# Kernel tuning notes

Hardware: AMD Instinct MI355X
Metric: run time of the kernel (lower is better)

Reference implementation:

```python
import jax, jax.numpy as jnp
import numpy as np

BLOCK_LEN = 64


def segsum(x):
    """x: (..., T) -> (..., T, T) with segsum[i,j] = sum_{k=j+1..i} x[k] (lower-tri incl diag), -inf above."""
    T = x.shape[-1]
    xc = jnp.cumsum(x, axis=-1)
    seg = xc[..., :, None] - xc[..., None, :]
    mask = jnp.tril(jnp.ones((T, T), dtype=bool))
    return jnp.where(mask, seg, -jnp.inf)


def setup_inputs() -> dict:
    key = jax.random.key(0)
    kx, ka, kb, kc = jax.random.split(key, 4)
    b, s, h, p, n = 4, 4096, 32, 64, 64
    X = jax.random.normal(kx, (b, s, h), dtype=jnp.float32)  # placeholder to keep split order stable
    X = jax.random.normal(kx, (b, s, h, p), dtype=jnp.float32)
    # A must be negative for a stable SSM decay (exp of cumulative sums stays bounded)
    A = -jax.random.uniform(ka, (b, s, h), dtype=jnp.float32, minval=0.0, maxval=1.0)
    B = jax.random.normal(kb, (b, s, h, n), dtype=jnp.float32)
    C = jax.random.normal(kc, (b, s, h, n), dtype=jnp.float32)
    return {"X": X, "A": A, "B": B, "C": C}


def reference(X, A, B, C):
    blk = BLOCK_LEN
    b, s, h, p = X.shape
    n = B.shape[-1]
    c = s // blk
    # chunk: b (c l) ... -> b c l ...
    Xc = X.reshape(b, c, blk, h, p)
    Bc = B.reshape(b, c, blk, h, n)
    Cc = C.reshape(b, c, blk, h, n)
    Ac = A.reshape(b, c, blk, h).transpose(0, 3, 1, 2)  # b h c l
    A_cumsum = jnp.cumsum(Ac, axis=-1)                  # b h c l

    # 1. intra-chunk (diagonal block) output
    L = jnp.exp(segsum(Ac))                             # b h c l s
    Y_diag = jnp.einsum("bclhn,bcshn,bhcls,bcshp->bclhp", Cc, Bc, L, Xc)

    # 2. intra-chunk states (chunk-final state assuming zero initial state)
    decay_states = jnp.exp(A_cumsum[..., -1:] - A_cumsum)
    states = jnp.einsum("bclhn,bhcl,bclhp->bchpn", Bc, decay_states, Xc)

    # 3. inter-chunk recurrence over chunk boundaries
    init = jnp.zeros_like(states[:, :1])
    states = jnp.concatenate([init, states], axis=1)    # b (c+1) h p n
    A_last = jnp.pad(A_cumsum[..., -1], ((0, 0), (0, 0), (1, 0)))  # b h (c+1)
    decay_chunk = jnp.exp(segsum(A_last))               # b h (c+1) (c+1)
    new_states = jnp.einsum("bhzc,bchpn->bzhpn", decay_chunk, states)
    states_in = new_states[:, :-1]                      # state entering each chunk

    # 4. state -> output
    state_decay_out = jnp.exp(A_cumsum)
    Y_off = jnp.einsum("bclhn,bchpn,bhcl->bclhp", Cc, states_in, state_decay_out)

    Y = (Y_diag + Y_off).reshape(b, s, h, p)
    return Y
```

## Files before the change

### kernel.cpp

```cpp
#include <hip/hip_runtime.h>

namespace {

typedef __attribute__((ext_vector_type(8))) short short8;
typedef __attribute__((ext_vector_type(4))) float f32x4;

constexpr int Hh = 32;
constexpr int Ss = 4096;
constexpr int HP = 64;
constexpr int HN = 64;
constexpr int NCH = 64;
constexpr int SB = 72;
constexpr int SS = 68;

__device__ inline unsigned short f2bf(float f) {
  unsigned u = __float_as_uint(f);
  u += 0x7FFFu + ((u >> 16) & 1u);
  return (unsigned short)(u >> 16);
}
__device__ inline float bf2f(unsigned short s) {
  return __uint_as_float(((unsigned)s) << 16);
}

__global__ __launch_bounds__(512, 1)
void ssd_mfma(const float* __restrict__ Xg0, const float* __restrict__ Ag0,
              const float* __restrict__ Bg0, const float* __restrict__ Cg0,
              float* __restrict__ Yg0) {
  __shared__ unsigned short Cs[2][64 * SB];
  __shared__ unsigned short Bs[2][64 * SB];
  __shared__ unsigned short BT[2][64 * SB];
  __shared__ unsigned short XT[2][32 * SB];
  __shared__ unsigned short Gs[64 * SB];
  __shared__ float STs[32 * SS];
  __shared__ float ac[2][64];

  const int tid = threadIdx.x;
  const int blk = blockIdx.x;
  const int ph = blk & 1;
  const int hi = (blk >> 1) & 31;
  const int bi = blk >> 6;

  const float* Xg = Xg0 + ((size_t)bi * Ss * Hh + hi) * HP + ph * 32;
  const float* Bg = Bg0 + ((size_t)bi * Ss * Hh + hi) * HN;
  const float* Cg = Cg0 + ((size_t)bi * Ss * Hh + hi) * HN;
  const float* Ag = Ag0 + (size_t)bi * Ss * Hh + hi;
  float*       Yg = Yg0 + ((size_t)bi * Ss * Hh + hi) * HP + ph * 32;

  const int w = tid >> 6, lane = tid & 63;
  const int lr = lane & 15, lk = lane >> 4;

  for (int i = tid; i < 32 * SS; i += 512) STs[i] = 0.f;

  float4 rb0, rb1, rc0, rc1, rx0;

  auto stage_load = [&](int ci) {
    const size_t rB = (size_t)ci * 64;
    const int r = tid >> 4, c = (tid & 15) * 4;
    rb0 = *(const float4*)(Bg + (rB + r) * (Hh * HN) + c);
    rc0 = *(const float4*)(Cg + (rB + r) * (Hh * HN) + c);
    rb1 = *(const float4*)(Bg + (rB + r + 32) * (Hh * HN) + c);
    rc1 = *(const float4*)(Cg + (rB + r + 32) * (Hh * HN) + c);
    const int rx = tid >> 3, cx = (tid & 7) * 4;
    rx0 = *(const float4*)(Xg + (rB + rx) * (Hh * HP) + cx);
  };

  auto stage_write = [&](int buf) {
    unsigned short* bs = Bs[buf];
    unsigned short* cs = Cs[buf];
    unsigned short* bt = BT[buf];
    unsigned short* xt = XT[buf];
    const int r = tid >> 4, c = (tid & 15) * 4;
    unsigned short b0[4] = {f2bf(rb0.x), f2bf(rb0.y), f2bf(rb0.z), f2bf(rb0.w)};
    unsigned short b1[4] = {f2bf(rb1.x), f2bf(rb1.y), f2bf(rb1.z), f2bf(rb1.w)};
    unsigned short c0[4] = {f2bf(rc0.x), f2bf(rc0.y), f2bf(rc0.z), f2bf(rc0.w)};
    unsigned short c1[4] = {f2bf(rc1.x), f2bf(rc1.y), f2bf(rc1.z), f2bf(rc1.w)};
    *(uint2*)&bs[r * SB + c]        = *(const uint2*)b0;
    *(uint2*)&bs[(r + 32) * SB + c] = *(const uint2*)b1;
    *(uint2*)&cs[r * SB + c]        = *(const uint2*)c0;
    *(uint2*)&cs[(r + 32) * SB + c] = *(const uint2*)c1;
#pragma unroll
    for (int j = 0; j < 4; ++j) {
      bt[(c + j) * SB + r]      = b0[j];
      bt[(c + j) * SB + r + 32] = b1[j];
    }
    const int rx = tid >> 3, cx = (tid & 7) * 4;
    unsigned short x0[4] = {f2bf(rx0.x), f2bf(rx0.y), f2bf(rx0.z), f2bf(rx0.w)};
#pragma unroll
    for (int j = 0; j < 4; ++j) xt[(cx + j) * SB + rx] = x0[j];
  };

  auto a_scan = [&](int ci) {
    if (tid < 64) {
      float a = Ag[(size_t)(ci * 64 + tid) * Hh];
#pragma unroll
      for (int off = 1; off < 64; off <<= 1) {
        float v = __shfl_up(a, off);
        if (tid >= off) a += v;
      }
      ac[ci & 1][tid] = a;
    }
  };

  stage_load(0);
  stage_write(0);
  a_scan(0);

  for (int ci = 0; ci < NCH; ++ci) {
    const int cur = ci & 1;
    __syncthreads();

    if (ci + 1 < NCH) {
      stage_load(ci + 1);
      a_scan(ci + 1);
    }

    const unsigned short* cs = Cs[cur];
    const unsigned short* bs = Bs[cur];
    const unsigned short* bt = BT[cur];
    const unsigned short* xt = XT[cur];
    const float* acv = ac[cur];
    const size_t rB = (size_t)ci * 64;

    {
      const int tl = w >> 1;
#pragma unroll
      for (int t = 0; t < 2; ++t) {
        const int ts = (w & 1) * 2 + t;
        if (ts > tl) {
#pragma unroll
          for (int i = 0; i < 4; ++i)
            Gs[(tl * 16 + lk * 4 + i) * SB + ts * 16 + lr] = 0;
        } else {
          f32x4 acc = {0.f, 0.f, 0.f, 0.f};
#pragma unroll
          for (int ks = 0; ks < 2; ++ks) {
            short8 a = *(const short8*)&cs[(tl * 16 + lr) * SB + ks * 32 + lk * 8];
            short8 b = *(const short8*)&bs[(ts * 16 + lr) * SB + ks * 32 + lk * 8];
            acc = __builtin_amdgcn_mfma_f32_16x16x32_bf16(a, b, acc, 0, 0, 0);
          }
          const int gcol = ts * 16 + lr;
          const float acol = acv[gcol];
#pragma unroll
          for (int i = 0; i < 4; ++i) {
            const int grow = tl * 16 + lk * 4 + i;
            float g = (gcol <= grow) ? acc[i] * __expf(acv[grow] - acol) : 0.f;
            Gs[grow * SB + gcol] = f2bf(g);
          }
        }
      }
    }
    __syncthreads();

    {
      const int tl = w >> 1, tp = w & 1;
      f32x4 aD = {0.f, 0.f, 0.f, 0.f};
      f32x4 aO = {0.f, 0.f, 0.f, 0.f};
#pragma unroll
      for (int ks = 0; ks < 2; ++ks) {
        const int ko = ks * 32 + lk * 8;
        short8 g = *(const short8*)&Gs[(tl * 16 + lr) * SB + ko];
        short8 x = *(const short8*)&xt[(tp * 16 + lr) * SB + ko];
        aD = __builtin_amdgcn_mfma_f32_16x16x32_bf16(g, x, aD, 0, 0, 0);
        short8 c8 = *(const short8*)&cs[(tl * 16 + lr) * SB + ko];
        const float* srow = &STs[(tp * 16 + lr) * SS + ko];
        float4 s0 = *(const float4*)srow;
        float4 s1 = *(const float4*)(srow + 4);
        short8 sb;
        sb[0] = (short)f2bf(s0.x); sb[1] = (short)f2bf(s0.y);
        sb[2] = (short)f2bf(s0.z); sb[3] = (short)f2bf(s0.w);
        sb[4] = (short)f2bf(s1.x); sb[5] = (short)f2bf(s1.y);
        sb[6] = (short)f2bf(s1.z); sb[7] = (short)f2bf(s1.w);
        aO = __builtin_amdgcn_mfma_f32_16x16x32_bf16(c8, sb, aO, 0, 0, 0);
      }
#pragma unroll
      for (int i = 0; i < 4; ++i) {
        const int grow = tl * 16 + lk * 4 + i;
        const float el = __expf(acv[grow]);
        Yg[(rB + grow) * (Hh * HP) + tp * 16 + lr] = aD[i] + el * aO[i];
      }
    }
    __syncthreads();

    {
      const int tp = w >> 2, tn = w & 3;
      const float atot = acv[63];
      f32x4 acc = {0.f, 0.f, 0.f, 0.f};
#pragma unroll
      for (int ks = 0; ks < 2; ++ks) {
        const int ko = ks * 32 + lk * 8;
        short8 a = *(const short8*)&xt[(tp * 16 + lr) * SB + ko];
        short8 braw = *(const short8*)&bt[(tn * 16 + lr) * SB + ko];
        short8 bsc;
#pragma unroll
        for (int j = 0; j < 8; ++j) {
          const float dl = __expf(atot - acv[ko + j]);
          bsc[j] = (short)f2bf(bf2f((unsigned short)braw[j]) * dl);
        }
        acc = __builtin_amdgcn_mfma_f32_16x16x32_bf16(a, bsc, acc, 0, 0, 0);
      }
      const float ea = __expf(atot);
#pragma unroll
      for (int i = 0; i < 4; ++i) {
        const int p = tp * 16 + lk * 4 + i, n = tn * 16 + lr;
        STs[p * SS + n] = STs[p * SS + n] * ea + acc[i];
      }
    }

    if (ci + 1 < NCH) stage_write((ci + 1) & 1);
  }
}

}

extern "C" void kernel_launch(void* const* d_in, const int* in_sizes, int n_in,
                              void* d_out, int out_size, void* d_ws, size_t ws_size,
                              hipStream_t stream) {
  const float* X = (const float*)d_in[0];
  const float* A = (const float*)d_in[1];
  const float* B = (const float*)d_in[2];
  const float* C = (const float*)d_in[3];
  float* Y = (float*)d_out;
  (void)d_ws; (void)ws_size; (void)in_sizes; (void)n_in; (void)out_size;
  ssd_mfma<<<dim3(256), dim3(512), 0, stream>>>(X, A, B, C, Y);
}
```

Baseline: 236.7 us.

## Split warps into diag and state-update groups with prescaled B and register state

```diff
diff --git a/kernel.cpp b/kernel.cpp
--- a/kernel.cpp
+++ b/kernel.cpp
@@ -5,40 +5,50 @@
 typedef __attribute__((ext_vector_type(8))) short short8;
 typedef __attribute__((ext_vector_type(4))) float f32x4;
 
-constexpr int Hh = 32;
-constexpr int Ss = 4096;
-constexpr int HP = 64;
-constexpr int HN = 64;
-constexpr int NCH = 64;
-constexpr int SB = 72;
-constexpr int SS = 68;
+constexpr int Hh = 32, Ss = 4096, HP = 64, HN = 64, NCH = 64;
+constexpr int ST = 68;
 
 __device__ inline unsigned short f2bf(float f) {
   unsigned u = __float_as_uint(f);
   u += 0x7FFFu + ((u >> 16) & 1u);
   return (unsigned short)(u >> 16);
 }
-__device__ inline float bf2f(unsigned short s) {
-  return __uint_as_float(((unsigned)s) << 16);
-}
-
-__global__ __launch_bounds__(512, 1)
-void ssd_mfma(const float* __restrict__ Xg0, const float* __restrict__ Ag0,
-              const float* __restrict__ Bg0, const float* __restrict__ Cg0,
-              float* __restrict__ Yg0) {
-  __shared__ unsigned short Cs[2][64 * SB];
-  __shared__ unsigned short Bs[2][64 * SB];
-  __shared__ unsigned short BT[2][64 * SB];
-  __shared__ unsigned short XT[2][32 * SB];
-  __shared__ unsigned short Gs[64 * SB];
-  __shared__ float STs[32 * SS];
-  __shared__ float ac[2][64];
+
+__device__ inline short8 frag(const unsigned short* p) {
+  union { short8 s; uint2 u[2]; } r;
+  r.u[0] = *(const uint2*)p;
+  r.u[1] = *(const uint2*)(p + 4);
+  return r.s;
+}
+
+__device__ inline uint2 cvt4(float4 v) {
+  uint2 o; unsigned short* s = (unsigned short*)&o;
+  s[0] = f2bf(v.x); s[1] = f2bf(v.y); s[2] = f2bf(v.z); s[3] = f2bf(v.w);
+  return o;
+}
+
+__device__ inline uint2 sxor8(uint2 v) {
+  uint2 o;
+  o.x = (unsigned)__shfl_xor((int)v.x, 8);
+  o.y = (unsigned)__shfl_xor((int)v.y, 8);
+  return o;
+}
+
+__global__ __launch_bounds__(1024, 4)
+void ssd4(const float* __restrict__ Xg0, const float* __restrict__ Ag0,
+          const float* __restrict__ Bg0, const float* __restrict__ Cg0,
+          float* __restrict__ Yg0) {
+  __shared__ unsigned short Bs[2][64 * ST];
+  __shared__ unsigned short Cs[2][64 * ST];
+  __shared__ unsigned short BT[2][64 * ST];
+  __shared__ unsigned short XT[2][32 * ST];
+  __shared__ unsigned short Gs[64 * ST];
+  __shared__ unsigned short Sb[2][32 * ST];
+  __shared__ float elt[4][64], ielt[4][64];
 
   const int tid = threadIdx.x;
-  const int blk = blockIdx.x;
-  const int ph = blk & 1;
-  const int hi = (blk >> 1) & 31;
-  const int bi = blk >> 6;
+  const int blk = ((blockIdx.x & 7) << 5) | (blockIdx.x >> 3);
+  const int ph = blk & 1, hi = (blk >> 1) & 31, bi = blk >> 6;
 
   const float* Xg = Xg0 + ((size_t)bi * Ss * Hh + hi) * HP + ph * 32;
   const float* Bg = Bg0 + ((size_t)bi * Ss * Hh + hi) * HN;
@@ -49,45 +59,14 @@
   const int w = tid >> 6, lane = tid & 63;
   const int lr = lane & 15, lk = lane >> 4;
 
-  for (int i = tid; i < 32 * SS; i += 512) STs[i] = 0.f;
-
-  float4 rb0, rb1, rc0, rc1, rx0;
-
-  auto stage_load = [&](int ci) {
-    const size_t rB = (size_t)ci * 64;
-    const int r = tid >> 4, c = (tid & 15) * 4;
-    rb0 = *(const float4*)(Bg + (rB + r) * (Hh * HN) + c);
-    rc0 = *(const float4*)(Cg + (rB + r) * (Hh * HN) + c);
-    rb1 = *(const float4*)(Bg + (rB + r + 32) * (Hh * HN) + c);
-    rc1 = *(const float4*)(Cg + (rB + r + 32) * (Hh * HN) + c);
-    const int rx = tid >> 3, cx = (tid & 7) * 4;
-    rx0 = *(const float4*)(Xg + (rB + rx) * (Hh * HP) + cx);
-  };
-
-  auto stage_write = [&](int buf) {
-    unsigned short* bs = Bs[buf];
-    unsigned short* cs = Cs[buf];
-    unsigned short* bt = BT[buf];
-    unsigned short* xt = XT[buf];
-    const int r = tid >> 4, c = (tid & 15) * 4;
-    unsigned short b0[4] = {f2bf(rb0.x), f2bf(rb0.y), f2bf(rb0.z), f2bf(rb0.w)};
-    unsigned short b1[4] = {f2bf(rb1.x), f2bf(rb1.y), f2bf(rb1.z), f2bf(rb1.w)};
-    unsigned short c0[4] = {f2bf(rc0.x), f2bf(rc0.y), f2bf(rc0.z), f2bf(rc0.w)};
-    unsigned short c1[4] = {f2bf(rc1.x), f2bf(rc1.y), f2bf(rc1.z), f2bf(rc1.w)};
-    *(uint2*)&bs[r * SB + c]        = *(const uint2*)b0;
-    *(uint2*)&bs[(r + 32) * SB + c] = *(const uint2*)b1;
-    *(uint2*)&cs[r * SB + c]        = *(const uint2*)c0;
-    *(uint2*)&cs[(r + 32) * SB + c] = *(const uint2*)c1;
-#pragma unroll
-    for (int j = 0; j < 4; ++j) {
-      bt[(c + j) * SB + r]      = b0[j];
-      bt[(c + j) * SB + r + 32] = b1[j];
-    }
-    const int rx = tid >> 3, cx = (tid & 7) * 4;
-    unsigned short x0[4] = {f2bf(rx0.x), f2bf(rx0.y), f2bf(rx0.z), f2bf(rx0.w)};
-#pragma unroll
-    for (int j = 0; j < 4; ++j) xt[(cx + j) * SB + rx] = x0[j];
-  };
+  const int tlA[8] = {0, 1, 1, 2, 2, 2, 3, 3};
+  const int tsA[8] = {0, 0, 1, 0, 1, 2, 0, 2};
+  const int ntA[8] = {1, 1, 1, 1, 1, 1, 2, 2};
+
+  for (int i = tid; i < 64 * ST; i += 1024) Gs[i] = 0;
+  for (int i = tid; i < 32 * ST; i += 1024) { Sb[0][i] = 0; Sb[1][i] = 0; }
+
+  float4 rA, rB2, rC1, rC2;
 
   auto a_scan = [&](int ci) {
     if (tid < 64) {
@@ -97,116 +76,149 @@
         float v = __shfl_up(a, off);
         if (tid >= off) a += v;
       }
-      ac[ci & 1][tid] = a;
+      elt[ci & 3][tid] = __expf(a);
+      ielt[ci & 3][tid] = __expf(-a);
     }
   };
 
+  auto stage_load = [&](int ci) {
+    const size_t rowB = (size_t)ci * 64;
+    if (w >= 8) {
+      const int u = tid - 512;
+      const int r = u >> 3, c = (u & 7) * 4;
+      const float* bp = Bg + (rowB + r) * (size_t)(Hh * HN);
+      const float* cp = Cg + (rowB + r) * (size_t)(Hh * HN);
+      rA  = *(const float4*)(bp + c);
+      rB2 = *(const float4*)(bp + c + 32);
+      rC1 = *(const float4*)(cp + c);
+      rC2 = *(const float4*)(cp + c + 32);
+    } else {
+      const int r = tid >> 3, c = (tid & 7) * 4;
+      rA = *(const float4*)(Xg + (rowB + r) * (size_t)(Hh * HP) + c);
+    }
+  };
+
+  auto stage_write = [&](int ci) {
+    const int buf = ci & 1, nb = ci & 3;
+    if (w >= 8) {
+      const int u = tid - 512;
+      const int r = u >> 3, c = (u & 7) * 4;
+      const float sc = ielt[nb][r];
+      float4 s1 = rA;  s1.x *= sc; s1.y *= sc; s1.z *= sc; s1.w *= sc;
+      float4 s2 = rB2; s2.x *= sc; s2.y *= sc; s2.z *= sc; s2.w *= sc;
+      uint2 t1 = cvt4(s1), t2 = cvt4(s2);
+      *(uint2*)&Bs[buf][r * ST + c]      = t1;
+      *(uint2*)&Bs[buf][r * ST + c + 32] = t2;
+      *(uint2*)&Cs[buf][r * ST + c]      = cvt4(rC1);
+      *(uint2*)&Cs[buf][r * ST + c + 32] = cvt4(rC2);
+      uint2 u1 = sxor8(t1), u2 = sxor8(t2);
+      const unsigned short* m1 = (const unsigned short*)&t1;
+      const unsigned short* p1 = (const unsigned short*)&u1;
+      const unsigned short* m2 = (const unsigned short*)&t2;
+      const unsigned short* p2 = (const unsigned short*)&u2;
+      const int g = r & 1, re = r & ~1;
+#pragma unroll
+      for (int jj = 0; jj < 2; ++jj) {
+        const int j = g * 2 + jj;
+        unsigned lo1 = g ? p1[j] : m1[j], hi1 = g ? m1[j] : p1[j];
+        unsigned lo2 = g ? p2[j] : m2[j], hi2 = g ? m2[j] : p2[j];
+        *(unsigned*)&BT[buf][(c + j) * ST + re]      = lo1 | (hi1 << 16);
+        *(unsigned*)&BT[buf][(c + 32 + j) * ST + re] = lo2 | (hi2 << 16);
+      }
+    } else {
+      const int r = tid >> 3, c = (tid & 7) * 4;
+      uint2 t1 = cvt4(rA);
+      uint2 u1 = sxor8(t1);
+      const unsigned short* m1 = (const unsigned short*)&t1;
+      const unsigned short* p1 = (const unsigned short*)&u1;
+      const int g = r & 1, re = r & ~1;
+#pragma unroll
+      for (int jj = 0; jj < 2; ++jj) {
+        const int j = g * 2 + jj;
+        unsigned lo = g ? p1[j] : m1[j], hi = g ? m1[j] : p1[j];
+        *(unsigned*)&XT[buf][(c + j) * ST + re] = lo | (hi << 16);
+      }
+    }
+  };
+
+  a_scan(0);
+  a_scan(1);
+  __syncthreads();
   stage_load(0);
   stage_write(0);
-  a_scan(0);
+  f32x4 Sreg = {0.f, 0.f, 0.f, 0.f};
 
   for (int ci = 0; ci < NCH; ++ci) {
     const int cur = ci & 1;
     __syncthreads();
-
-    if (ci + 1 < NCH) {
-      stage_load(ci + 1);
-      a_scan(ci + 1);
-    }
-
-    const unsigned short* cs = Cs[cur];
-    const unsigned short* bs = Bs[cur];
-    const unsigned short* bt = BT[cur];
-    const unsigned short* xt = XT[cur];
-    const float* acv = ac[cur];
-    const size_t rB = (size_t)ci * 64;
-
-    {
-      const int tl = w >> 1;
+    if (ci + 1 < NCH) stage_load(ci + 1);
+    if (ci + 2 < NCH) a_scan(ci + 2);
+
+    if (w < 8) {
+      const int tl = tlA[w];
+      const float* el = elt[ci & 3];
 #pragma unroll
       for (int t = 0; t < 2; ++t) {
-        const int ts = (w & 1) * 2 + t;
-        if (ts > tl) {
-#pragma unroll
-          for (int i = 0; i < 4; ++i)
-            Gs[(tl * 16 + lk * 4 + i) * SB + ts * 16 + lr] = 0;
-        } else {
-          f32x4 acc = {0.f, 0.f, 0.f, 0.f};
-#pragma unroll
-          for (int ks = 0; ks < 2; ++ks) {
-            short8 a = *(const short8*)&cs[(tl * 16 + lr) * SB + ks * 32 + lk * 8];
-            short8 b = *(const short8*)&bs[(ts * 16 + lr) * SB + ks * 32 + lk * 8];
-            acc = __builtin_amdgcn_mfma_f32_16x16x32_bf16(a, b, acc, 0, 0, 0);
-          }
-          const int gcol = ts * 16 + lr;
-          const float acol = acv[gcol];
-#pragma unroll
-          for (int i = 0; i < 4; ++i) {
-            const int grow = tl * 16 + lk * 4 + i;
-            float g = (gcol <= grow) ? acc[i] * __expf(acv[grow] - acol) : 0.f;
-            Gs[grow * SB + gcol] = f2bf(g);
-          }
+        if (t >= ntA[w]) break;
+        const int ts = tsA[w] + t;
+        f32x4 acc = {0.f, 0.f, 0.f, 0.f};
+#pragma unroll
+        for (int ks = 0; ks < 2; ++ks) {
+          short8 a = frag(&Cs[cur][(tl * 16 + lr) * ST + ks * 32 + lk * 8]);
+          short8 b = frag(&Bs[cur][(ts * 16 + lr) * ST + ks * 32 + lk * 8]);
+          acc = __builtin_amdgcn_mfma_f32_16x16x32_bf16(a, b, acc, 0, 0, 0);
         }
-      }
-    }
+        const int gcol = ts * 16 + lr;
+#pragma unroll
+        for (int i = 0; i < 4; ++i) {
+          const int grow = tl * 16 + lk * 4 + i;
+          float gv = (gcol <= grow) ? acc[i] * el[grow] : 0.f;
+          Gs[grow * ST + gcol] = f2bf(gv);
+        }
+      }
+    } else {
+      const int u = w - 8, tp = u >> 2, tn = u & 3;
+      f32x4 acc = Sreg;
+#pragma unroll
+      for (int ks = 0; ks < 2; ++ks) {
+        short8 a = frag(&XT[cur][(tp * 16 + lr) * ST + ks * 32 + lk * 8]);
+        short8 b = frag(&BT[cur][(tn * 16 + lr) * ST + ks * 32 + lk * 8]);
+        acc = __builtin_amdgcn_mfma_f32_16x16x32_bf16(a, b, acc, 0, 0, 0);
+      }
+      const float ea = elt[ci & 3][63];
+#pragma unroll
+      for (int i = 0; i < 4; ++i) acc[i] *= ea;
+      Sreg = acc;
+#pragma unroll
+      for (int i = 0; i < 4; ++i)
+        Sb[(ci + 1) & 1][(tp * 16 + lk * 4 + i) * ST + tn * 16 + lr] = f2bf(acc[i]);
+    }
+
     __syncthreads();
 
-    {
+    if (w < 8) {
       const int tl = w >> 1, tp = w & 1;
-      f32x4 aD = {0.f, 0.f, 0.f, 0.f};
-      f32x4 aO = {0.f, 0.f, 0.f, 0.f};
+      const size_t rB0 = (size_t)ci * 64;
+      f32x4 aD = {0.f, 0.f, 0.f, 0.f}, aO = {0.f, 0.f, 0.f, 0.f};
 #pragma unroll
       for (int ks = 0; ks < 2; ++ks) {
         const int ko = ks * 32 + lk * 8;
-        short8 g = *(const short8*)&Gs[(tl * 16 + lr) * SB + ko];
-        short8 x = *(const short8*)&xt[(tp * 16 + lr) * SB + ko];
-        aD = __builtin_amdgcn_mfma_f32_16x16x32_bf16(g, x, aD, 0, 0, 0);
-        short8 c8 = *(const short8*)&cs[(tl * 16 + lr) * SB + ko];
-        const float* srow = &STs[(tp * 16 + lr) * SS + ko];
-        float4 s0 = *(const float4*)srow;
-        float4 s1 = *(const float4*)(srow + 4);
-        short8 sb;
-        sb[0] = (short)f2bf(s0.x); sb[1] = (short)f2bf(s0.y);
-        sb[2] = (short)f2bf(s0.z); sb[3] = (short)f2bf(s0.w);
-        sb[4] = (short)f2bf(s1.x); sb[5] = (short)f2bf(s1.y);
-        sb[6] = (short)f2bf(s1.z); sb[7] = (short)f2bf(s1.w);
-        aO = __builtin_amdgcn_mfma_f32_16x16x32_bf16(c8, sb, aO, 0, 0, 0);
-      }
+        short8 gf = frag(&Gs[(tl * 16 + lr) * ST + ko]);
+        short8 xf = frag(&XT[cur][(tp * 16 + lr) * ST + ko]);
+        aD = __builtin_amdgcn_mfma_f32_16x16x32_bf16(gf, xf, aD, 0, 0, 0);
+        short8 cf = frag(&Cs[cur][(tl * 16 + lr) * ST + ko]);
+        short8 sf = frag(&Sb[cur][(tp * 16 + lr) * ST + ko]);
+        aO = __builtin_amdgcn_mfma_f32_16x16x32_bf16(cf, sf, aO, 0, 0, 0);
+      }
+      const float* el = elt[ci & 3];
 #pragma unroll
       for (int i = 0; i < 4; ++i) {
-        const int grow = tl * 16 + lk * 4 + i;
-        const float el = __expf(acv[grow]);
-        Yg[(rB + grow) * (Hh * HP) + tp * 16 + lr] = aD[i] + el * aO[i];
-      }
-    }
-    __syncthreads();
-
-    {
-      const int tp = w >> 2, tn = w & 3;
-      const float atot = acv[63];
-      f32x4 acc = {0.f, 0.f, 0.f, 0.f};
-#pragma unroll
-      for (int ks = 0; ks < 2; ++ks) {
-        const int ko = ks * 32 + lk * 8;
-        short8 a = *(const short8*)&xt[(tp * 16 + lr) * SB + ko];
-        short8 braw = *(const short8*)&bt[(tn * 16 + lr) * SB + ko];
-        short8 bsc;
-#pragma unroll
-        for (int j = 0; j < 8; ++j) {
-          const float dl = __expf(atot - acv[ko + j]);
-          bsc[j] = (short)f2bf(bf2f((unsigned short)braw[j]) * dl);
-        }
-        acc = __builtin_amdgcn_mfma_f32_16x16x32_bf16(a, bsc, acc, 0, 0, 0);
-      }
-      const float ea = __expf(atot);
-#pragma unroll
-      for (int i = 0; i < 4; ++i) {
-        const int p = tp * 16 + lk * 4 + i, n = tn * 16 + lr;
-        STs[p * SS + n] = STs[p * SS + n] * ea + acc[i];
-      }
-    }
-
-    if (ci + 1 < NCH) stage_write((ci + 1) & 1);
+        const int row = tl * 16 + lk * 4 + i;
+        Yg[(rB0 + row) * (size_t)(Hh * HP) + tp * 16 + lr] = aD[i] + el[row] * aO[i];
+      }
+    }
+
+    if (ci + 1 < NCH) stage_write(ci + 1);
   }
 }
 
@@ -221,5 +233,5 @@
   const float* C = (const float*)d_in[3];
   float* Y = (float*)d_out;
   (void)d_ws; (void)ws_size; (void)in_sizes; (void)n_in; (void)out_size;
-  ssd_mfma<<<dim3(256), dim3(512), 0, stream>>>(X, A, B, C, Y);
-}
+  ssd4<<<dim3(256), dim3(1024), 0, stream>>>(X, A, B, C, Y);
+}
```

After: 347.0 us. 46.6% more time.
